# Optimization experiments

Hardware: AMD Instinct MI355X
Metric: run time of the kernel (lower is better)

## Reference

```python
import jax, jax.numpy as jnp
import numpy as np

B = 131072          # batch of 128-bit plaintexts
N_ROUNDS = 10
C_PARAM = 1.0
SBOX_H = 32         # hidden width of the S-box emulating relu MLP (apply_op)


def setup_inputs() -> dict:
    key = jax.random.key(0)
    k0, k1, k2, k3, k4 = jax.random.split(key, 5)
    # binary plaintexts, batch x 128
    state_tensor = (jax.random.uniform(k0, (B, 128)) < 0.5).astype(jnp.float32)
    # round keys as binary states: [n_rounds+1, 1, 4, 4, 8] (broadcast over batch)
    round_keys = (jax.random.uniform(k1, (N_ROUNDS + 1, 1, 4, 4, 8)) < 0.5).astype(jnp.float32)
    # XOR-gadget weights: relu(a-b)+relu(b-a) == a XOR b on bits, scaled by c
    c = C_PARAM
    xorw = jnp.array([[c, -c], [-c, c]], dtype=jnp.float32)
    xorb = jnp.zeros((2,), dtype=jnp.float32)
    # SubBytes emulation weights (apply_op: relu(linear) -> linear on 8-bit bytes)
    sbox_w0 = jax.random.normal(k2, (SBOX_H, 8), dtype=jnp.float32) * 0.5
    sbox_b0 = jax.random.normal(k3, (SBOX_H,), dtype=jnp.float32) * 0.1
    sbox_w1 = jax.random.normal(k4, (8, SBOX_H), dtype=jnp.float32) * 0.5
    return {"state_tensor": state_tensor, "round_keys": round_keys,
            "xorw": xorw, "xorb": xorb,
            "sbox_w0": sbox_w0, "sbox_b0": sbox_b0, "sbox_w1": sbox_w1}


def _relu(x):
    return jnp.maximum(x, 0.0)


def reference(state_tensor, round_keys, xorw, xorb, sbox_w0, sbox_b0, sbox_w1):
    def ark(s, k):
        c0 = xorw[0, 0] * s + xorw[0, 1] * k + xorb[0]
        c1 = xorw[1, 0] * s + xorw[1, 1] * k + xorb[1]
        return _relu(c0) + _relu(c1)

    def sub_bytes(x):  # apply_op with w1: relu(linear) -> linear, per byte (last dim 8)
        h = _relu(jnp.einsum('bijk,hk->bijh', x, sbox_w0) + sbox_b0)
        return jnp.einsum('bijh,kh->bijk', h, sbox_w1)

    def shift_rows(x):  # roll row r by r along the column axis
        return jnp.stack([jnp.roll(x[:, :, r, :], -r, axis=1) for r in range(4)], axis=2)

    def mix_columns(x):  # XOR-of-3 across rows via the relu parity (xor4-style) gadget
        s = x + jnp.roll(x, -1, axis=2) + jnp.roll(x, -2, axis=2)
        return _relu(s) - 2.0 * _relu(s - 1.0) + 2.0 * _relu(s - 2.0) - 2.0 * _relu(s - 3.0)

    def aes_round(x, final=False):
        x = sub_bytes(x)
        x = shift_rows(x)
        if not final:
            x = mix_columns(x)
        return x

    # [B,128] -> [B,4,4,8], transpose(1,2)
    st = state_tensor.reshape(-1, 4, 4, 8).swapaxes(1, 2)
    st = ark(st, round_keys[0])
    for r in range(1, N_ROUNDS):
        st = aes_round(st)
        st = ark(st, round_keys[r])
    st = aes_round(st, final=True)
    st = ark(st, round_keys[N_ROUNDS])
    return st.swapaxes(1, 2).reshape(-1, 128)
```

## Files before the change

### kernel.cpp

```cpp
#include <hip/hip_runtime.h>

#define NH 32

__device__ __forceinline__ float mixg(float s) {
    float t0 = fmaxf(s, 0.f);
    float t1 = fmaxf(s - 1.f, 0.f);
    float t2 = fmaxf(s - 2.f, 0.f);
    float t3 = fmaxf(s - 3.f, 0.f);
    return t0 - 2.f * (t1 - t2 + t3);
}

struct alignas(16) SW {
    float w0[NH][8];
    float w1t[NH][8];
    float b0[NH];
    float pad[24];
    float t0[11 * 128];
    float t1[11 * 128];
};

template<int J0>
__device__ __forceinline__ void sub_group(float (&st)[4][4][8], const SW& sw)
{
    float acc[4][2][8];
    #pragma unroll
    for (int i = 0; i < 4; ++i)
        #pragma unroll
        for (int jj = 0; jj < 2; ++jj)
            #pragma unroll
            for (int k = 0; k < 8; ++k) acc[i][jj][k] = 0.f;

    for (int h = 0; h < NH; ++h) {
        float4 wa = *(const float4*)&sw.w0[h][0];
        float4 wb = *(const float4*)&sw.w0[h][4];
        float4 va = *(const float4*)&sw.w1t[h][0];
        float4 vb = *(const float4*)&sw.w1t[h][4];
        float bb = sw.b0[h];
        float wr[8] = {wa.x, wa.y, wa.z, wa.w, wb.x, wb.y, wb.z, wb.w};
        float vr[8] = {va.x, va.y, va.z, va.w, vb.x, vb.y, vb.z, vb.w};
        #pragma unroll
        for (int i = 0; i < 4; ++i) {
            #pragma unroll
            for (int jj = 0; jj < 2; ++jj) {
                float hv = bb;
                #pragma unroll
                for (int k = 0; k < 8; ++k) hv = fmaf(wr[k], st[i][J0 + jj][k], hv);
                hv = fmaxf(hv, 0.f);
                #pragma unroll
                for (int k = 0; k < 8; ++k) acc[i][jj][k] = fmaf(vr[k], hv, acc[i][jj][k]);
            }
        }
    }
    #pragma unroll
    for (int i = 0; i < 4; ++i)
        #pragma unroll
        for (int jj = 0; jj < 2; ++jj)
            #pragma unroll
            for (int k = 0; k < 8; ++k) st[i][J0 + jj][k] = acc[i][jj][k];
}

__global__ __launch_bounds__(256, 2) void neural_aes_kernel(
    const float* __restrict__ st_in,
    const float* __restrict__ rk,
    const float* __restrict__ xw,
    const float* __restrict__ xb,
    const float* __restrict__ w0,
    const float* __restrict__ b0,
    const float* __restrict__ w1,
    float* __restrict__ out, int B)
{
    __shared__ SW sw;
    const int tid = threadIdx.x;
    const float w00 = xw[0], w01 = xw[1], w10 = xw[2], w11 = xw[3];
    const float xb0 = xb[0], xb1 = xb[1];

    for (int idx = tid; idx < NH * 8; idx += 256) {
        int h = idx >> 3, k = idx & 7;
        sw.w0[h][k]  = w0[idx];
        sw.w1t[h][k] = w1[k * NH + h];
    }
    if (tid < NH) sw.b0[tid] = b0[tid];
    for (int idx = tid; idx < 11 * 128; idx += 256) {
        float kv = rk[idx];
        sw.t0[idx] = fmaf(w01, kv, xb0);
        sw.t1[idx] = fmaf(w11, kv, xb1);
    }
    __syncthreads();

    const int b = blockIdx.x * 256 + tid;
    if (b >= B) return;
    const float* __restrict__ inp = st_in + (size_t)b * 128;
    float* __restrict__ op = out + (size_t)b * 128;

    float st[4][4][8];

    #pragma unroll
    for (int j = 0; j < 4; ++j) {
        #pragma unroll
        for (int i = 0; i < 4; ++i) {
            float4 a = *(const float4*)(inp + j * 32 + i * 8);
            float4 c = *(const float4*)(inp + j * 32 + i * 8 + 4);
            float xv[8] = {a.x, a.y, a.z, a.w, c.x, c.y, c.z, c.w};
            #pragma unroll
            for (int k = 0; k < 8; ++k) {
                float t0v = sw.t0[i * 32 + j * 8 + k];
                float t1v = sw.t1[i * 32 + j * 8 + k];
                float c0 = fmaf(w00, xv[k], t0v);
                float c1 = fmaf(w10, xv[k], t1v);
                st[i][j][k] = fmaxf(c0, 0.f) + fmaxf(c1, 0.f);
            }
        }
    }

    for (int r = 1; r <= 9; ++r) {
        sub_group<0>(st, sw);
        sub_group<2>(st, sw);

        #pragma unroll
        for (int k = 0; k < 8; ++k) {
            float ns[4][4];
            #pragma unroll
            for (int i = 0; i < 4; ++i) {
                #pragma unroll
                for (int j = 0; j < 4; ++j) {
                    float s = st[(i + j) & 3][j][k]
                            + st[(i + j + 1) & 3][(j + 1) & 3][k]
                            + st[(i + j + 2) & 3][(j + 2) & 3][k];
                    ns[i][j] = mixg(s);
                }
            }
            #pragma unroll
            for (int i = 0; i < 4; ++i)
                #pragma unroll
                for (int j = 0; j < 4; ++j) st[i][j][k] = ns[i][j];
        }

        const float* t0p = sw.t0 + r * 128;
        const float* t1p = sw.t1 + r * 128;
        #pragma unroll
        for (int i = 0; i < 4; ++i) {
            #pragma unroll
            for (int j = 0; j < 4; ++j) {
                float4 ta = *(const float4*)(t0p + i * 32 + j * 8);
                float4 tb = *(const float4*)(t0p + i * 32 + j * 8 + 4);
                float4 ua = *(const float4*)(t1p + i * 32 + j * 8);
                float4 ub = *(const float4*)(t1p + i * 32 + j * 8 + 4);
                float tr0[8] = {ta.x, ta.y, ta.z, ta.w, tb.x, tb.y, tb.z, tb.w};
                float tr1[8] = {ua.x, ua.y, ua.z, ua.w, ub.x, ub.y, ub.z, ub.w};
                #pragma unroll
                for (int k = 0; k < 8; ++k) {
                    float c0 = fmaf(w00, st[i][j][k], tr0[k]);
                    float c1 = fmaf(w10, st[i][j][k], tr1[k]);
                    st[i][j][k] = fmaxf(c0, 0.f) + fmaxf(c1, 0.f);
                }
            }
        }
    }

    sub_group<0>(st, sw);
    sub_group<2>(st, sw);
    const float* t0p = sw.t0 + 10 * 128;
    const float* t1p = sw.t1 + 10 * 128;
    #pragma unroll
    for (int j = 0; j < 4; ++j) {
        #pragma unroll
        for (int i = 0; i < 4; ++i) {
            float4 ta = *(const float4*)(t0p + i * 32 + j * 8);
            float4 tb = *(const float4*)(t0p + i * 32 + j * 8 + 4);
            float4 ua = *(const float4*)(t1p + i * 32 + j * 8);
            float4 ub = *(const float4*)(t1p + i * 32 + j * 8 + 4);
            float tr0[8] = {ta.x, ta.y, ta.z, ta.w, tb.x, tb.y, tb.z, tb.w};
            float tr1[8] = {ua.x, ua.y, ua.z, ua.w, ub.x, ub.y, ub.z, ub.w};
            float v[8];
            #pragma unroll
            for (int k = 0; k < 8; ++k) {
                float x = st[(i + j) & 3][j][k];
                float c0 = fmaf(w00, x, tr0[k]);
                float c1 = fmaf(w10, x, tr1[k]);
                v[k] = fmaxf(c0, 0.f) + fmaxf(c1, 0.f);
            }
            float4 oa = {v[0], v[1], v[2], v[3]};
            float4 oc = {v[4], v[5], v[6], v[7]};
            *(float4*)(op + j * 32 + i * 8) = oa;
            *(float4*)(op + j * 32 + i * 8 + 4) = oc;
        }
    }
}

extern "C" void kernel_launch(void* const* d_in, const int* in_sizes, int n_in,
                              void* d_out, int out_size, void* d_ws, size_t ws_size,
                              hipStream_t stream) {
    const float* st_in = (const float*)d_in[0];
    const float* rk    = (const float*)d_in[1];
    const float* xw    = (const float*)d_in[2];
    const float* xb    = (const float*)d_in[3];
    const float* w0    = (const float*)d_in[4];
    const float* b0    = (const float*)d_in[5];
    const float* w1    = (const float*)d_in[6];
    float* out = (float*)d_out;
    const int B = in_sizes[0] / 128;
    const int grid = (B + 255) / 256;
    neural_aes_kernel<<<grid, 256, 0, stream>>>(st_in, rk, xw, xb, w0, b0, w1, out, B);
}
```

Baseline: 417.4 us.

## Move weights and key tables from LDS to global scalar loads via prep kernel

Adds a small prep kernel that transposes w1 and precomputes the key-XOR tables into the workspace. The main kernel drops its shared-memory staging and block barrier and reads the warp-uniform weights and tables straight from global memory, so the compiler can use scalar (SGPR) loads instead of LDS reads in the hot S-box loop. The h-loop is unrolled by two and the occupancy hints move to amdgpu attributes. In exchange it adds a second launch, and it depends on the compiler proving the loads uniform and turning them into scalar loads, with constant-cache pressure possible.

```diff
diff --git a/kernel.cpp b/kernel.cpp
--- a/kernel.cpp
+++ b/kernel.cpp
@@ -1,6 +1,30 @@
 #include <hip/hip_runtime.h>
 
 #define NH 32
+
+#define WS_W1T 0
+#define WS_T0  256
+#define WS_T1  1664
+
+__global__ __launch_bounds__(256) void prep_kernel(
+    const float* __restrict__ rk,
+    const float* __restrict__ xw,
+    const float* __restrict__ xb,
+    const float* __restrict__ w1,
+    float* __restrict__ ws)
+{
+    const int idx = blockIdx.x * 256 + threadIdx.x;
+    const float w01 = xw[1], w11 = xw[3], xb0 = xb[0], xb1 = xb[1];
+    if (idx < NH * 8) {
+        int h = idx >> 3, k = idx & 7;
+        ws[WS_W1T + idx] = w1[k * NH + h];
+    }
+    if (idx < 11 * 128) {
+        float kv = rk[idx];
+        ws[WS_T0 + idx] = fmaf(w01, kv, xb0);
+        ws[WS_T1 + idx] = fmaf(w11, kv, xb1);
+    }
+}
 
 __device__ __forceinline__ float mixg(float s) {
     float t0 = fmaxf(s, 0.f);
@@ -10,17 +34,11 @@
     return t0 - 2.f * (t1 - t2 + t3);
 }
 
-struct alignas(16) SW {
-    float w0[NH][8];
-    float w1t[NH][8];
-    float b0[NH];
-    float pad[24];
-    float t0[11 * 128];
-    float t1[11 * 128];
-};
-
 template<int J0>
-__device__ __forceinline__ void sub_group(float (&st)[4][4][8], const SW& sw)
+__device__ __forceinline__ void sub_group(float (&st)[4][4][8],
+                                          const float* __restrict__ w0g,
+                                          const float* __restrict__ b0g,
+                                          const float* __restrict__ w1tg)
 {
     float acc[4][2][8];
     #pragma unroll
@@ -30,14 +48,11 @@
             #pragma unroll
             for (int k = 0; k < 8; ++k) acc[i][jj][k] = 0.f;
 
+    #pragma unroll 2
     for (int h = 0; h < NH; ++h) {
-        float4 wa = *(const float4*)&sw.w0[h][0];
-        float4 wb = *(const float4*)&sw.w0[h][4];
-        float4 va = *(const float4*)&sw.w1t[h][0];
-        float4 vb = *(const float4*)&sw.w1t[h][4];
-        float bb = sw.b0[h];
-        float wr[8] = {wa.x, wa.y, wa.z, wa.w, wb.x, wb.y, wb.z, wb.w};
-        float vr[8] = {va.x, va.y, va.z, va.w, vb.x, vb.y, vb.z, vb.w};
+        const float* __restrict__ wr = w0g + h * 8;
+        const float* __restrict__ vr = w1tg + h * 8;
+        const float bb = b0g[h];
         #pragma unroll
         for (int i = 0; i < 4; ++i) {
             #pragma unroll
@@ -59,35 +74,22 @@
             for (int k = 0; k < 8; ++k) st[i][J0 + jj][k] = acc[i][jj][k];
 }
 
-__global__ __launch_bounds__(256, 2) void neural_aes_kernel(
+__global__ __attribute__((amdgpu_flat_work_group_size(256, 256),
+                          amdgpu_waves_per_eu(2, 2)))
+void neural_aes_kernel(
     const float* __restrict__ st_in,
-    const float* __restrict__ rk,
     const float* __restrict__ xw,
-    const float* __restrict__ xb,
-    const float* __restrict__ w0,
-    const float* __restrict__ b0,
-    const float* __restrict__ w1,
+    const float* __restrict__ w0g,
+    const float* __restrict__ b0g,
+    const float* __restrict__ wsg,
     float* __restrict__ out, int B)
 {
-    __shared__ SW sw;
-    const int tid = threadIdx.x;
-    const float w00 = xw[0], w01 = xw[1], w10 = xw[2], w11 = xw[3];
-    const float xb0 = xb[0], xb1 = xb[1];
+    const float w00 = xw[0], w10 = xw[2];
+    const float* __restrict__ w1tg = wsg + WS_W1T;
+    const float* __restrict__ t0g  = wsg + WS_T0;
+    const float* __restrict__ t1g  = wsg + WS_T1;
 
-    for (int idx = tid; idx < NH * 8; idx += 256) {
-        int h = idx >> 3, k = idx & 7;
-        sw.w0[h][k]  = w0[idx];
-        sw.w1t[h][k] = w1[k * NH + h];
-    }
-    if (tid < NH) sw.b0[tid] = b0[tid];
-    for (int idx = tid; idx < 11 * 128; idx += 256) {
-        float kv = rk[idx];
-        sw.t0[idx] = fmaf(w01, kv, xb0);
-        sw.t1[idx] = fmaf(w11, kv, xb1);
-    }
-    __syncthreads();
-
-    const int b = blockIdx.x * 256 + tid;
+    const int b = blockIdx.x * 256 + threadIdx.x;
     if (b >= B) return;
     const float* __restrict__ inp = st_in + (size_t)b * 128;
     float* __restrict__ op = out + (size_t)b * 128;
@@ -103,18 +105,16 @@
             float xv[8] = {a.x, a.y, a.z, a.w, c.x, c.y, c.z, c.w};
             #pragma unroll
             for (int k = 0; k < 8; ++k) {
-                float t0v = sw.t0[i * 32 + j * 8 + k];
-                float t1v = sw.t1[i * 32 + j * 8 + k];
-                float c0 = fmaf(w00, xv[k], t0v);
-                float c1 = fmaf(w10, xv[k], t1v);
+                float c0 = fmaf(w00, xv[k], t0g[i * 32 + j * 8 + k]);
+                float c1 = fmaf(w10, xv[k], t1g[i * 32 + j * 8 + k]);
                 st[i][j][k] = fmaxf(c0, 0.f) + fmaxf(c1, 0.f);
             }
         }
     }
 
     for (int r = 1; r <= 9; ++r) {
-        sub_group<0>(st, sw);
-        sub_group<2>(st, sw);
+        sub_group<0>(st, w0g, b0g, w1tg);
+        sub_group<2>(st, w0g, b0g, w1tg);
 
         #pragma unroll
         for (int k = 0; k < 8; ++k) {
@@ -135,48 +135,36 @@
                 for (int j = 0; j < 4; ++j) st[i][j][k] = ns[i][j];
         }
 
-        const float* t0p = sw.t0 + r * 128;
-        const float* t1p = sw.t1 + r * 128;
+        const float* __restrict__ t0p = t0g + r * 128;
+        const float* __restrict__ t1p = t1g + r * 128;
         #pragma unroll
         for (int i = 0; i < 4; ++i) {
             #pragma unroll
             for (int j = 0; j < 4; ++j) {
-                float4 ta = *(const float4*)(t0p + i * 32 + j * 8);
-                float4 tb = *(const float4*)(t0p + i * 32 + j * 8 + 4);
-                float4 ua = *(const float4*)(t1p + i * 32 + j * 8);
-                float4 ub = *(const float4*)(t1p + i * 32 + j * 8 + 4);
-                float tr0[8] = {ta.x, ta.y, ta.z, ta.w, tb.x, tb.y, tb.z, tb.w};
-                float tr1[8] = {ua.x, ua.y, ua.z, ua.w, ub.x, ub.y, ub.z, ub.w};
                 #pragma unroll
                 for (int k = 0; k < 8; ++k) {
-                    float c0 = fmaf(w00, st[i][j][k], tr0[k]);
-                    float c1 = fmaf(w10, st[i][j][k], tr1[k]);
+                    float c0 = fmaf(w00, st[i][j][k], t0p[i * 32 + j * 8 + k]);
+                    float c1 = fmaf(w10, st[i][j][k], t1p[i * 32 + j * 8 + k]);
                     st[i][j][k] = fmaxf(c0, 0.f) + fmaxf(c1, 0.f);
                 }
             }
         }
     }
 
-    sub_group<0>(st, sw);
-    sub_group<2>(st, sw);
-    const float* t0p = sw.t0 + 10 * 128;
-    const float* t1p = sw.t1 + 10 * 128;
+    sub_group<0>(st, w0g, b0g, w1tg);
+    sub_group<2>(st, w0g, b0g, w1tg);
+    const float* __restrict__ t0p = t0g + 10 * 128;
+    const float* __restrict__ t1p = t1g + 10 * 128;
     #pragma unroll
     for (int j = 0; j < 4; ++j) {
         #pragma unroll
         for (int i = 0; i < 4; ++i) {
-            float4 ta = *(const float4*)(t0p + i * 32 + j * 8);
-            float4 tb = *(const float4*)(t0p + i * 32 + j * 8 + 4);
-            float4 ua = *(const float4*)(t1p + i * 32 + j * 8);
-            float4 ub = *(const float4*)(t1p + i * 32 + j * 8 + 4);
-            float tr0[8] = {ta.x, ta.y, ta.z, ta.w, tb.x, tb.y, tb.z, tb.w};
-            float tr1[8] = {ua.x, ua.y, ua.z, ua.w, ub.x, ub.y, ub.z, ub.w};
             float v[8];
             #pragma unroll
             for (int k = 0; k < 8; ++k) {
                 float x = st[(i + j) & 3][j][k];
-                float c0 = fmaf(w00, x, tr0[k]);
-                float c1 = fmaf(w10, x, tr1[k]);
+                float c0 = fmaf(w00, x, t0p[i * 32 + j * 8 + k]);
+                float c1 = fmaf(w10, x, t1p[i * 32 + j * 8 + k]);
                 v[k] = fmaxf(c0, 0.f) + fmaxf(c1, 0.f);
             }
             float4 oa = {v[0], v[1], v[2], v[3]};
@@ -198,7 +186,9 @@
     const float* b0    = (const float*)d_in[5];
     const float* w1    = (const float*)d_in[6];
     float* out = (float*)d_out;
+    float* ws  = (float*)d_ws;
     const int B = in_sizes[0] / 128;
-    const int grid = (B + 255) / 256;
-    neural_aes_kernel<<<grid, 256, 0, stream>>>(st_in, rk, xw, xb, w0, b0, w1, out, B);
+
+    prep_kernel<<<6, 256, 0, stream>>>(rk, xw, xb, w1, ws);
+    neural_aes_kernel<<<(B + 255) / 256, 256, 0, stream>>>(st_in, xw, w0, b0, ws, out, B);
 }
```

New measurement: 446.0 us. 1.07x slower.
